# Performance work log

Measured on AMD Instinct MI355X. Metric: run time of the kernel, lower is better.

Reference implementation:

```python
import jax, jax.numpy as jnp
import numpy as np

# Production-scale graph dims (see shape_source)
N = 50000      # nodes
E = 800000     # edges (avg degree 16)
C_IN = 128     # input feature dim
H = 96         # hidden (per species: prey X and predator Y)
C_OUT = 40     # num_classes
L = 5          # LVConv layers
DT = 0.05      # integration step


def setup_inputs() -> dict:
    key = jax.random.key(0)
    ks = jax.random.split(key, 14)
    x = jax.random.normal(ks[0], (N, C_IN), jnp.float32)
    edge_index = jax.random.randint(ks[1], (2, E), 0, N, dtype=jnp.int32)
    # lift linears
    Wx = jax.random.normal(ks[2], (C_IN, H), jnp.float32) / np.sqrt(C_IN)
    bx = jnp.zeros((H,), jnp.float32)
    Wy = jax.random.normal(ks[3], (C_IN, H), jnp.float32) / np.sqrt(C_IN)
    by = jnp.zeros((H,), jnp.float32)
    # per-layer Lotka-Volterra coefficients (per-channel), small positive scale
    alpha = 0.1 * jax.random.uniform(ks[4], (L, H), jnp.float32)
    beta  = 0.1 * jax.random.uniform(ks[5], (L, H), jnp.float32)
    gamma = 0.1 * jax.random.uniform(ks[6], (L, H), jnp.float32)
    delta = 0.1 * jax.random.uniform(ks[7], (L, H), jnp.float32)
    # readout on concat([X, Y])
    Wr = jax.random.normal(ks[8], (2 * H, C_OUT), jnp.float32) / np.sqrt(2 * H)
    br = jnp.zeros((C_OUT,), jnp.float32)
    return {"x": x, "edge_index": edge_index, "Wx": Wx, "bx": bx,
            "Wy": Wy, "by": by, "alpha": alpha, "beta": beta,
            "gamma": gamma, "delta": delta, "Wr": Wr, "br": br}


def reference(x, edge_index, Wx, bx, Wy, by, alpha, beta, gamma, delta, Wr, br):
    src, dst = edge_index[0], edge_index[1]
    # in-degree for mean aggregation over incoming edges
    deg = jax.ops.segment_sum(jnp.ones((E,), x.dtype), dst, num_segments=N)
    deg_inv = (1.0 / jnp.maximum(deg, 1.0))[:, None]  # [N,1]

    def mean_agg(v):  # [N,H] -> [N,H] neighbor mean (src -> dst)
        return jax.ops.segment_sum(v[src], dst, num_segments=N) * deg_inv

    # lift to prey (X) and predator (Y) populations
    X = jnp.tanh(x @ Wx + bx)
    Y = jnp.tanh(x @ Wy + by)
    # dropout is identity in eval mode (training=False)
    for l in range(L):
        aggX = mean_agg(X)
        aggY = mean_agg(Y)
        # explicit-Euler Lotka-Volterra dynamics on the graph
        Xn = X + DT * X * (alpha[l] - beta[l] * aggY)
        Yn = Y + DT * Y * (-gamma[l] + delta[l] * aggX)
        X, Y = Xn, Yn
    h = jnp.concatenate([X, Y], axis=-1)  # [N, 2H]
    return h @ Wr + br
```

## Files before the change

kernel.cpp:

```cpp
#include <hip/hip_runtime.h>
#include <hip/hip_bf16.h>
#include <hip/hip_fp16.h>


#define HDIM 96
#define CIN 128
#define COUT 40
#define NLAYER 5
#define DTC 0.05f

#define BK_SHIFT 7
#define BK_SIZE 128
#define EPB 2048
#define BCAP 3072
#define BSTRIDE 3584

typedef float  vfloat2 __attribute__((ext_vector_type(2)));
typedef float  vfloat4 __attribute__((ext_vector_type(4)));
typedef short  vshort8 __attribute__((ext_vector_type(8)));

__device__ __forceinline__ unsigned bf16_rne(float f) {
    unsigned u = __float_as_uint(f);
    return (u + 0x7fffu + ((u >> 16) & 1u)) >> 16;
}

__device__ __forceinline__ unsigned pack_bf16_pair(float xf, float yf) {
    return bf16_rne(xf) | (bf16_rne(yf) << 16);
}

__device__ __forceinline__ unsigned pack_f16_pair(float a, float b) {
    unsigned ha = (unsigned)__half_as_ushort(__float2half_rn(a));
    unsigned hb = (unsigned)__half_as_ushort(__float2half_rn(b));
    return ha | (hb << 16);
}

__device__ __forceinline__ float f16_lo(unsigned u) {
    return __half2float(__ushort_as_half((unsigned short)(u & 0xffffu)));
}
__device__ __forceinline__ float f16_hi(unsigned u) {
    return __half2float(__ushort_as_half((unsigned short)(u >> 16)));
}

__device__ __forceinline__ unsigned pack_fp8_quad(float x0, float y0, float x1, float y1) {
    int lo = __builtin_amdgcn_cvt_pk_fp8_f32(x0, y0, 0, false);
    int full = __builtin_amdgcn_cvt_pk_fp8_f32(x1, y1, lo, true);
    return (unsigned)full;
}

__device__ __forceinline__ float fast_tanh(float x) {
    float e = __expf(2.0f * x);
    return 1.0f - 2.0f * __builtin_amdgcn_rcpf(e + 1.0f);
}


__global__ __launch_bounds__(256) void wprep_kernel(
    const float* __restrict__ Wx, const float* __restrict__ bx,
    const float* __restrict__ Wy, const float* __restrict__ by,
    unsigned short* __restrict__ WcT, float* __restrict__ bc,
    int* __restrict__ gcur, int NB,
    unsigned* __restrict__ F0, unsigned* __restrict__ F1, int N) {
    int t = blockIdx.x * blockDim.x + threadIdx.x;
    if (t < NB) gcur[t] = 0;
    if (t < 192 * 128) {
        int cc = t >> 7;
        int k = t & 127;
        int h = cc >> 1;
        float w = (cc & 1) ? Wy[k * HDIM + h] : Wx[k * HDIM + h];
        WcT[cc * 128 + k] = (unsigned short)bf16_rne(w);
    }
    if (t < 192) {
        int h = t >> 1;
        bc[t] = (t & 1) ? by[h] : bx[h];
    }
    if (blockIdx.x == 0 && threadIdx.x < 48) {
        int plane = threadIdx.x >> 4, d = threadIdx.x & 15;
        size_t o = ((size_t)plane * (N + 1) + N) * 16 + d;
        F0[o] = 0u;
        F1[o] = 0u;
    }
}


__global__ __launch_bounds__(256) void bscatter_kernel(
    const int* __restrict__ src, const int* __restrict__ dst,
    int* __restrict__ gcur, unsigned* __restrict__ packed, int E, int NB) {
    __shared__ int h[512];
    __shared__ int cur[512];
    for (int i = threadIdx.x; i < NB; i += 256) h[i] = 0;
    __syncthreads();
    int base = blockIdx.x * EPB;
    int end = min(E, base + EPB);
    for (int e = base + threadIdx.x; e < end; e += 256)
        atomicAdd(&h[dst[e] >> BK_SHIFT], 1);
    __syncthreads();
    for (int i = threadIdx.x; i < NB; i += 256)
        cur[i] = h[i] ? atomicAdd(&gcur[i], h[i]) : 0;
    __syncthreads();
    for (int e = base + threadIdx.x; e < end; e += 256) {
        int d = dst[e];
        int b = d >> BK_SHIFT;
        int pos = atomicAdd(&cur[b], 1);
        if (pos < BCAP)
            packed[(size_t)b * BCAP + pos] =
                (unsigned)src[e] | ((unsigned)(d & (BK_SIZE - 1)) << 17);
    }
}


__global__ __launch_bounds__(256) void bcsr_kernel(
    const unsigned* __restrict__ packed, const int* __restrict__ gcur,
    uint2* __restrict__ rowinfo, int* __restrict__ csr, int N, int NB) {
    __shared__ int ldeg[BK_SIZE];
    __shared__ int sscan[BK_SIZE];
    __shared__ int lcur[BK_SIZE];
    int b = blockIdx.x;
    int t = threadIdx.x;
    int cnt = min(gcur[b], BCAP);
    const unsigned* pk = packed + (size_t)b * BCAP;
    int wbase = b * BSTRIDE;
    if (t < BK_SIZE) ldeg[t] = 0;
    __syncthreads();
    for (int e = t; e < cnt; e += 256)
        atomicAdd(&ldeg[(pk[e] >> 17) & (BK_SIZE - 1)], 1);
    __syncthreads();
    int deg = 0, pad = 0;
    if (t < BK_SIZE) {
        deg = ldeg[t];
        pad = (deg + 3) & ~3;
        sscan[t] = pad;
    }
    __syncthreads();
    for (int off = 1; off < BK_SIZE; off <<= 1) {
        int tv = (t < BK_SIZE && t >= off) ? sscan[t - off] : 0;
        __syncthreads();
        if (t < BK_SIZE) sscan[t] += tv;
        __syncthreads();
    }
    int gpos = 0;
    if (t < BK_SIZE) {
        gpos = wbase + sscan[t] - pad;
        lcur[t] = gpos;
        int node = b * BK_SIZE + t;
        if (node < N) {
            rowinfo[node] = make_uint2(
                (unsigned)gpos | ((unsigned)(pad >> 2) << 21),
                __float_as_uint(1.0f / fmaxf((float)deg, 1.0f)));
        }
    }
    __syncthreads();
    for (int e = t; e < cnt; e += 256) {
        unsigned p = pk[e];
        int l = (p >> 17) & (BK_SIZE - 1);
        int pos = atomicAdd(&lcur[l], 1);
        csr[pos] = (int)(p & 0x1FFFFu);
    }
    __syncthreads();
    if (t < BK_SIZE) {
        for (int p = lcur[t]; p < gpos + pad; p++) csr[p] = N;
    }
}


#define LW_STRIDE 136
#define TILE_STRIDE 200

__global__ __launch_bounds__(256) void lift_mfma_kernel(
    const float* __restrict__ x, const unsigned short* __restrict__ WcT,
    const float* __restrict__ bc, unsigned* __restrict__ S,
    unsigned* __restrict__ F, int N) {
    __shared__ __align__(16) char smem[192 * LW_STRIDE * 2];
    __shared__ float sBc[192];
    unsigned short* sW = (unsigned short*)smem;
    unsigned short* tile = (unsigned short*)smem;
    int t = threadIdx.x;

    {
        const unsigned* g = (const unsigned*)WcT;
        unsigned* s = (unsigned*)sW;
        for (int i = t; i < 192 * 64; i += 256) {
            int cc = i >> 6;
            int kp = i & 63;
            s[cc * (LW_STRIDE / 2) + kp] = g[i];
        }
    }
    if (t < 192) sBc[t] = bc[t];
    __syncthreads();

    int wv = t >> 6;
    int lane = t & 63;
    int quad = lane >> 4;
    int m = lane & 15;
    int mbase = blockIdx.x * 64 + wv * 16;

    int anode = mbase + m;
    if (anode >= N) anode = N - 1;
    const float* xrow = x + (size_t)anode * CIN;

    vfloat4 acc[12];
#pragma unroll
    for (int i = 0; i < 12; i++) acc[i] = (vfloat4){0.f, 0.f, 0.f, 0.f};

#pragma unroll
    for (int kt = 0; kt < 4; kt++) {
        int k0 = kt * 32 + quad * 8;
        float4 xa = *(const float4*)(xrow + k0);
        float4 xb = *(const float4*)(xrow + k0 + 4);
        uint4 ua;
        ua.x = pack_bf16_pair(xa.x, xa.y);
        ua.y = pack_bf16_pair(xa.z, xa.w);
        ua.z = pack_bf16_pair(xb.x, xb.y);
        ua.w = pack_bf16_pair(xb.z, xb.w);
        vshort8 a = *(vshort8*)&ua;
#pragma unroll
        for (int nt = 0; nt < 12; nt++) {
            vshort8 b = *(const vshort8*)&sW[(nt * 16 + m) * LW_STRIDE + k0];
            acc[nt] = __builtin_amdgcn_mfma_f32_16x16x32_bf16(a, b, acc[nt], 0, 0, 0);
        }
    }

    __syncthreads();
#pragma unroll
    for (int nt = 0; nt < 12; nt++) {
        int ccb = nt * 16 + m;
        float bco = sBc[ccb];
#pragma unroll
        for (int r = 0; r < 4; r++) {
            int nl = wv * 16 + quad * 4 + r;
            float v = fast_tanh(acc[nt][r] + bco);
            tile[nl * TILE_STRIDE + ccb] = __half_as_ushort(__float2half_rn(v));
        }
    }
    __syncthreads();

    int nbase = blockIdx.x * 64;
#pragma unroll
    for (int i = 0; i < 6; i++) {
        int idx = i * 256 + t;
        int nl = idx / 24;
        int pos = idx - nl * 24;
        int node = nbase + nl;
        uint4 u = *(const uint4*)&tile[nl * TILE_STRIDE + pos * 8];
        if (node < N) {
            *(uint4*)(S + (size_t)node * 96 + pos * 4) = u;
            float f0 = f16_lo(u.x), f1 = f16_hi(u.x);
            float f2 = f16_lo(u.y), f3 = f16_hi(u.y);
            float f4 = f16_lo(u.z), f5 = f16_hi(u.z);
            float f6 = f16_lo(u.w), f7 = f16_hi(u.w);
            uint2 fq = make_uint2(pack_fp8_quad(f0, f1, f2, f3),
                                  pack_fp8_quad(f4, f5, f6, f7));
            int plane = pos >> 3;
            int slot = (2 * pos) & 15;
            *(uint2*)(F + ((size_t)plane * (N + 1) + node) * 16 + slot) = fq;
        }
    }
}


__global__ __launch_bounds__(256) void layer_kernel(
    const unsigned* __restrict__ F, const unsigned* __restrict__ S,
    unsigned* __restrict__ Sn, unsigned* __restrict__ Fn,
    const uint2* __restrict__ rowinfo, const int* __restrict__ csr,
    const float* __restrict__ alpha, const float* __restrict__ beta,
    const float* __restrict__ gamma, const float* __restrict__ delta,
    int N, int nblk) {
    int bid = blockIdx.x;
    int plane = bid / nblk;
    int tile = bid - plane * nblk;
    size_t pstride = (size_t)(N + 1) * 16;
    const unsigned* Fp = F + (size_t)plane * pstride;

    int wave = threadIdx.x >> 6;
    int lane = threadIdx.x & 63;
    int li = lane & 15;
    int gbase = lane & 48;

    int node = (tile * 4 + wave) * 4 + (lane >> 4);
    bool nvalid = node < N;
    int nclamp = nvalid ? node : N - 1;
    uint2 ri = rowinfo[nclamp];
    int beg = (int)(ri.x & 0x1FFFFFu);
    int cnt = nvalid ? (int)((ri.x >> 21) << 2) : 0;
    float dinv = __uint_as_float(ri.y);

    vfloat2 a0 = (vfloat2){0.f, 0.f};
    vfloat2 a1 = (vfloat2){0.f, 0.f};

#define UNP(u)                                                              \
    do {                                                                    \
        a0 += __builtin_amdgcn_cvt_pk_f32_fp8((int)(u), false);             \
        a1 += __builtin_amdgcn_cvt_pk_f32_fp8((int)(u), true);              \
    } while (0)

    for (int base = 0; base < cnt; base += 64) {
        int rem = min(cnt - base, 64);
        int4 my = {0, 0, 0, 0};
        if (li * 4 < rem) my = *(const int4*)(csr + beg + base + 4 * li);
        int j = 0;
        for (; j + 8 <= rem; j += 8) {
            int l0 = gbase + (j >> 2);
            int s0 = __shfl(my.x, l0);
            int s1 = __shfl(my.y, l0);
            int s2 = __shfl(my.z, l0);
            int s3 = __shfl(my.w, l0);
            int s4 = __shfl(my.x, l0 + 1);
            int s5 = __shfl(my.y, l0 + 1);
            int s6 = __shfl(my.z, l0 + 1);
            int s7 = __shfl(my.w, l0 + 1);
            unsigned u0 = Fp[(size_t)s0 * 16 + li];
            unsigned u1 = Fp[(size_t)s1 * 16 + li];
            unsigned u2 = Fp[(size_t)s2 * 16 + li];
            unsigned u3 = Fp[(size_t)s3 * 16 + li];
            unsigned u4 = Fp[(size_t)s4 * 16 + li];
            unsigned u5 = Fp[(size_t)s5 * 16 + li];
            unsigned u6 = Fp[(size_t)s6 * 16 + li];
            unsigned u7 = Fp[(size_t)s7 * 16 + li];
            UNP(u0); UNP(u1); UNP(u2); UNP(u3);
            UNP(u4); UNP(u5); UNP(u6); UNP(u7);
        }
        if (j < rem) {
            int l0 = gbase + (j >> 2);
            int s0 = __shfl(my.x, l0);
            int s1 = __shfl(my.y, l0);
            int s2 = __shfl(my.z, l0);
            int s3 = __shfl(my.w, l0);
            unsigned u0 = Fp[(size_t)s0 * 16 + li];
            unsigned u1 = Fp[(size_t)s1 * 16 + li];
            unsigned u2 = Fp[(size_t)s2 * 16 + li];
            unsigned u3 = Fp[(size_t)s3 * 16 + li];
            UNP(u0); UNP(u1); UNP(u2); UNP(u3);
        }
    }
#undef UNP

    if (!nvalid) return;

    int h0 = plane * 32 + 2 * li;
    float2 a2 = *(const float2*)(alpha + h0);
    float2 b2 = *(const float2*)(beta + h0);
    float2 g2 = *(const float2*)(gamma + h0);
    float2 d2 = *(const float2*)(delta + h0);
    uint2 su = *(const uint2*)(S + (size_t)node * 96 + h0);
    float vx = f16_lo(su.x), vy = f16_hi(su.x);
    float vz = f16_lo(su.y), vw = f16_hi(su.y);
    float ox = vx + DTC * vx * (a2.x - b2.x * (a0.y * dinv));
    float oy = vy + DTC * vy * (-g2.x + d2.x * (a0.x * dinv));
    float oz = vz + DTC * vz * (a2.y - b2.y * (a1.y * dinv));
    float ow = vw + DTC * vw * (-g2.y + d2.y * (a1.x * dinv));
    uint2 so = make_uint2(pack_f16_pair(ox, oy), pack_f16_pair(oz, ow));
    *(uint2*)(Sn + (size_t)node * 96 + h0) = so;
    if (Fn) Fn[(size_t)plane * pstride + (size_t)node * 16 + li] =
        pack_fp8_quad(ox, oy, oz, ow);
}


#define WG_STRIDE 200

__global__ __launch_bounds__(256) void readout_mfma_kernel(
    const unsigned short* __restrict__ sh, const float* __restrict__ Wr,
    const float* __restrict__ br, float* __restrict__ out, int N) {
    __shared__ unsigned short sW[48 * WG_STRIDE];
    __shared__ float sB[48];
    int t = threadIdx.x;

    for (int i = t; i < 48 * 192; i += 256) {
        int n = i / 192;
        int kk = i - n * 192;
        int h = kk >> 1;
        float w = 0.f;
        if (n < COUT) w = (kk & 1) ? Wr[(HDIM + h) * COUT + n] : Wr[h * COUT + n];
        sW[n * WG_STRIDE + kk] = __half_as_ushort(__float2half_rn(w));
    }
    if (t < 48) sB[t] = (t < COUT) ? br[t] : 0.f;
    __syncthreads();

    int wv = t >> 6;
    int lane = t & 63;
    int quad = lane >> 4;
    int m = lane & 15;
    int mbase = blockIdx.x * 64 + wv * 16;

    int anode = mbase + m;
    if (anode >= N) anode = N - 1;
    const unsigned short* arow = sh + (size_t)anode * 192;

    vfloat4 acc0 = {0.f, 0.f, 0.f, 0.f};
    vfloat4 acc1 = {0.f, 0.f, 0.f, 0.f};
    vfloat4 acc2 = {0.f, 0.f, 0.f, 0.f};

#pragma unroll
    for (int kt = 0; kt < 6; kt++) {
        int k0 = kt * 32 + quad * 8;
        vshort8 a = *(const vshort8*)(arow + k0);
        vshort8 b0 = *(const vshort8*)&sW[(0 * 16 + m) * WG_STRIDE + k0];
        vshort8 b1 = *(const vshort8*)&sW[(1 * 16 + m) * WG_STRIDE + k0];
        vshort8 b2 = *(const vshort8*)&sW[(2 * 16 + m) * WG_STRIDE + k0];
        acc0 = __builtin_amdgcn_mfma_f32_16x16x32_f16(a, b0, acc0, 0, 0, 0);
        acc1 = __builtin_amdgcn_mfma_f32_16x16x32_f16(a, b1, acc1, 0, 0, 0);
        acc2 = __builtin_amdgcn_mfma_f32_16x16x32_f16(a, b2, acc2, 0, 0, 0);
    }

    float bo0 = sB[m];
    float bo1 = sB[16 + m];
    float bo2 = (m < 8) ? sB[32 + m] : 0.f;
#pragma unroll
    for (int r = 0; r < 4; r++) {
        int node = mbase + quad * 4 + r;
        if (node < N) {
            float* orow = out + (size_t)node * COUT;
            orow[m] = acc0[r] + bo0;
            orow[16 + m] = acc1[r] + bo1;
            if (m < 8) orow[32 + m] = acc2[r] + bo2;
        }
    }
}


extern "C" void kernel_launch(void* const* d_in, const int* in_sizes, int n_in,
                              void* d_out, int out_size, void* d_ws, size_t ws_size,
                              hipStream_t stream) {
    const float* x     = (const float*)d_in[0];
    const int*   ei    = (const int*)d_in[1];
    const float* Wx    = (const float*)d_in[2];
    const float* bx    = (const float*)d_in[3];
    const float* Wy    = (const float*)d_in[4];
    const float* by    = (const float*)d_in[5];
    const float* alpha = (const float*)d_in[6];
    const float* beta  = (const float*)d_in[7];
    const float* gamma = (const float*)d_in[8];
    const float* delta = (const float*)d_in[9];
    const float* Wr    = (const float*)d_in[10];
    const float* br    = (const float*)d_in[11];

    const int N = in_sizes[0] / CIN;
    const int E = in_sizes[1] / 2;
    const int NB = (N + BK_SIZE - 1) >> BK_SHIFT;
    const int nchunk = (E + EPB - 1) / EPB;
    const int nblk = (N + 15) / 16;

    char* ws = (char*)d_ws;
    size_t off = 0;
    auto alloc = [&](size_t bytes) -> void* {
        off = (off + 255) & ~(size_t)255;
        void* p = ws + off;
        off += bytes;
        return p;
    };
    int* gcur          = (int*)alloc((size_t)NB * sizeof(int));
    unsigned* pckd     = (unsigned*)alloc((size_t)NB * BCAP * sizeof(unsigned));
    uint2* rowinfo     = (uint2*)alloc((size_t)N * sizeof(uint2));
    int* csr           = (int*)alloc(((size_t)NB * BSTRIDE + 64) * sizeof(int));
    unsigned* Sa   = (unsigned*)alloc((size_t)N * 96 * sizeof(unsigned));
    unsigned* Sb   = (unsigned*)alloc((size_t)N * 96 * sizeof(unsigned));
    unsigned* Fa   = (unsigned*)alloc((size_t)(N + 1) * 48 * sizeof(unsigned));
    unsigned* Fb   = (unsigned*)alloc((size_t)(N + 1) * 48 * sizeof(unsigned));
    unsigned short* WcT = (unsigned short*)alloc((size_t)192 * 128 * sizeof(unsigned short));
    float* bc      = (float*)alloc((size_t)192 * sizeof(float));
    (void)ws_size;

    const int* e_src = ei;
    const int* e_dst = ei + E;

    wprep_kernel<<<(192 * 128 + 255) / 256, 256, 0, stream>>>(
        Wx, bx, Wy, by, WcT, bc, gcur, NB, Fa, Fb, N);

    bscatter_kernel<<<nchunk, 256, 0, stream>>>(e_src, e_dst, gcur, pckd, E, NB);
    bcsr_kernel<<<NB, 256, 0, stream>>>(pckd, gcur, rowinfo, csr, N, NB);

    lift_mfma_kernel<<<(N + 63) / 64, 256, 0, stream>>>(x, WcT, bc, Sa, Fa, N);

    const unsigned* Sc = Sa;
    unsigned* Snx = Sb;
    const unsigned* Fc = Fa;
    unsigned* Fnx = Fb;
    for (int l = 0; l < NLAYER; l++) {
        bool last = (l == NLAYER - 1);
        layer_kernel<<<3 * nblk, 256, 0, stream>>>(
            Fc, Sc, Snx, last ? (unsigned*)nullptr : Fnx,
            rowinfo, csr,
            alpha + l * HDIM, beta + l * HDIM, gamma + l * HDIM, delta + l * HDIM,
            N, nblk);
        const unsigned* ts = Sc; Sc = Snx; Snx = (unsigned*)ts;
        const unsigned* tf = Fc; Fc = Fnx; Fnx = (unsigned*)tf;
    }

    readout_mfma_kernel<<<(N + 63) / 64, 256, 0, stream>>>(
        (const unsigned short*)Sc, Wr, br, (float*)d_out, N);
}
```

Measured before the change: 285.3 us.

## Use 16-bit CSR indices and 8-lane-per-node gathers with in-place state update

Neighbour indices are stored as unsigned shorts, and rows are padded to multiples of 8 so each node reads one 16-byte vector of 8 indices per step with no cross-lane shuffles. Each node is now handled by 8 lanes, each gathering 8 bytes of fp8 features per neighbour, so fewer load instructions are issued per edge and each block covers 32 nodes. The f16 state buffer is updated in place, which drops the second state buffer and its ping-pong. The 16-bit indices only hold for fewer than 65536 nodes, and padding to 8 adds some dummy gathers.

```diff
diff --git a/kernel.cpp b/kernel.cpp
--- a/kernel.cpp
+++ b/kernel.cpp
@@ -13,7 +13,7 @@
 #define BK_SIZE 128
 #define EPB 2048
 #define BCAP 3072
-#define BSTRIDE 3584
+#define BSTRIDE 4096
 
 typedef float  vfloat2 __attribute__((ext_vector_type(2)));
 typedef float  vfloat4 __attribute__((ext_vector_type(4)));
@@ -109,7 +109,7 @@
 
 __global__ __launch_bounds__(256) void bcsr_kernel(
     const unsigned* __restrict__ packed, const int* __restrict__ gcur,
-    uint2* __restrict__ rowinfo, int* __restrict__ csr, int N, int NB) {
+    uint2* __restrict__ rowinfo, unsigned short* __restrict__ csr, int N, int NB) {
     __shared__ int ldeg[BK_SIZE];
     __shared__ int sscan[BK_SIZE];
     __shared__ int lcur[BK_SIZE];
@@ -126,7 +126,7 @@
     int deg = 0, pad = 0;
     if (t < BK_SIZE) {
         deg = ldeg[t];
-        pad = (deg + 3) & ~3;
+        pad = (deg + 7) & ~7;
         sscan[t] = pad;
     }
     __syncthreads();
@@ -152,11 +152,11 @@
         unsigned p = pk[e];
         int l = (p >> 17) & (BK_SIZE - 1);
         int pos = atomicAdd(&lcur[l], 1);
-        csr[pos] = (int)(p & 0x1FFFFu);
+        csr[pos] = (unsigned short)(p & 0x1FFFFu);
     }
     __syncthreads();
     if (t < BK_SIZE) {
-        for (int p = lcur[t]; p < gpos + pad; p++) csr[p] = N;
+        for (int p = lcur[t]; p < gpos + pad; p++) csr[p] = (unsigned short)N;
     }
 }
 
@@ -257,99 +257,101 @@
 
 
 __global__ __launch_bounds__(256) void layer_kernel(
-    const unsigned* __restrict__ F, const unsigned* __restrict__ S,
-    unsigned* __restrict__ Sn, unsigned* __restrict__ Fn,
-    const uint2* __restrict__ rowinfo, const int* __restrict__ csr,
+    const unsigned* __restrict__ F, unsigned* __restrict__ S,
+    unsigned* __restrict__ Fn,
+    const uint2* __restrict__ rowinfo, const unsigned short* __restrict__ csr,
     const float* __restrict__ alpha, const float* __restrict__ beta,
     const float* __restrict__ gamma, const float* __restrict__ delta,
     int N, int nblk) {
     int bid = blockIdx.x;
     int plane = bid / nblk;
     int tile = bid - plane * nblk;
-    size_t pstride = (size_t)(N + 1) * 16;
+    unsigned pstride = (unsigned)(N + 1) * 16u;
     const unsigned* Fp = F + (size_t)plane * pstride;
 
     int wave = threadIdx.x >> 6;
     int lane = threadIdx.x & 63;
-    int li = lane & 15;
-    int gbase = lane & 48;
-
-    int node = (tile * 4 + wave) * 4 + (lane >> 4);
+    int li = lane & 7;
+    unsigned tli = (unsigned)(2 * li);
+
+    int node = tile * 32 + wave * 8 + (lane >> 3);
     bool nvalid = node < N;
     int nclamp = nvalid ? node : N - 1;
     uint2 ri = rowinfo[nclamp];
-    int beg = (int)(ri.x & 0x1FFFFFu);
+    unsigned beg = ri.x & 0x1FFFFFu;
     int cnt = nvalid ? (int)((ri.x >> 21) << 2) : 0;
     float dinv = __uint_as_float(ri.y);
 
-    vfloat2 a0 = (vfloat2){0.f, 0.f};
-    vfloat2 a1 = (vfloat2){0.f, 0.f};
+    vfloat2 a0 = {0.f, 0.f}, a1 = {0.f, 0.f}, a2 = {0.f, 0.f}, a3 = {0.f, 0.f};
 
 #define UNP(u)                                                              \
     do {                                                                    \
-        a0 += __builtin_amdgcn_cvt_pk_f32_fp8((int)(u), false);             \
-        a1 += __builtin_amdgcn_cvt_pk_f32_fp8((int)(u), true);              \
+        a0 += __builtin_amdgcn_cvt_pk_f32_fp8((int)(u).x, false);           \
+        a1 += __builtin_amdgcn_cvt_pk_f32_fp8((int)(u).x, true);            \
+        a2 += __builtin_amdgcn_cvt_pk_f32_fp8((int)(u).y, false);           \
+        a3 += __builtin_amdgcn_cvt_pk_f32_fp8((int)(u).y, true);            \
     } while (0)
 
-    for (int base = 0; base < cnt; base += 64) {
-        int rem = min(cnt - base, 64);
-        int4 my = {0, 0, 0, 0};
-        if (li * 4 < rem) my = *(const int4*)(csr + beg + base + 4 * li);
-        int j = 0;
-        for (; j + 8 <= rem; j += 8) {
-            int l0 = gbase + (j >> 2);
-            int s0 = __shfl(my.x, l0);
-            int s1 = __shfl(my.y, l0);
-            int s2 = __shfl(my.z, l0);
-            int s3 = __shfl(my.w, l0);
-            int s4 = __shfl(my.x, l0 + 1);
-            int s5 = __shfl(my.y, l0 + 1);
-            int s6 = __shfl(my.z, l0 + 1);
-            int s7 = __shfl(my.w, l0 + 1);
-            unsigned u0 = Fp[(size_t)s0 * 16 + li];
-            unsigned u1 = Fp[(size_t)s1 * 16 + li];
-            unsigned u2 = Fp[(size_t)s2 * 16 + li];
-            unsigned u3 = Fp[(size_t)s3 * 16 + li];
-            unsigned u4 = Fp[(size_t)s4 * 16 + li];
-            unsigned u5 = Fp[(size_t)s5 * 16 + li];
-            unsigned u6 = Fp[(size_t)s6 * 16 + li];
-            unsigned u7 = Fp[(size_t)s7 * 16 + li];
-            UNP(u0); UNP(u1); UNP(u2); UNP(u3);
-            UNP(u4); UNP(u5); UNP(u6); UNP(u7);
-        }
-        if (j < rem) {
-            int l0 = gbase + (j >> 2);
-            int s0 = __shfl(my.x, l0);
-            int s1 = __shfl(my.y, l0);
-            int s2 = __shfl(my.z, l0);
-            int s3 = __shfl(my.w, l0);
-            unsigned u0 = Fp[(size_t)s0 * 16 + li];
-            unsigned u1 = Fp[(size_t)s1 * 16 + li];
-            unsigned u2 = Fp[(size_t)s2 * 16 + li];
-            unsigned u3 = Fp[(size_t)s3 * 16 + li];
-            UNP(u0); UNP(u1); UNP(u2); UNP(u3);
-        }
+    for (int j = 0; j < cnt; j += 8) {
+        uint4 w = *(const uint4*)(csr + beg + (unsigned)j);
+        unsigned o0 = ((w.x & 0xffffu) << 4) + tli;
+        unsigned o1 = ((w.x >> 16) << 4) + tli;
+        unsigned o2 = ((w.y & 0xffffu) << 4) + tli;
+        unsigned o3 = ((w.y >> 16) << 4) + tli;
+        unsigned o4 = ((w.z & 0xffffu) << 4) + tli;
+        unsigned o5 = ((w.z >> 16) << 4) + tli;
+        unsigned o6 = ((w.w & 0xffffu) << 4) + tli;
+        unsigned o7 = ((w.w >> 16) << 4) + tli;
+        uint2 u0 = *(const uint2*)(Fp + o0);
+        uint2 u1 = *(const uint2*)(Fp + o1);
+        uint2 u2 = *(const uint2*)(Fp + o2);
+        uint2 u3 = *(const uint2*)(Fp + o3);
+        uint2 u4 = *(const uint2*)(Fp + o4);
+        uint2 u5 = *(const uint2*)(Fp + o5);
+        uint2 u6 = *(const uint2*)(Fp + o6);
+        uint2 u7 = *(const uint2*)(Fp + o7);
+        UNP(u0); UNP(u1); UNP(u2); UNP(u3);
+        UNP(u4); UNP(u5); UNP(u6); UNP(u7);
     }
 #undef UNP
 
     if (!nvalid) return;
 
-    int h0 = plane * 32 + 2 * li;
-    float2 a2 = *(const float2*)(alpha + h0);
-    float2 b2 = *(const float2*)(beta + h0);
-    float2 g2 = *(const float2*)(gamma + h0);
-    float2 d2 = *(const float2*)(delta + h0);
-    uint2 su = *(const uint2*)(S + (size_t)node * 96 + h0);
-    float vx = f16_lo(su.x), vy = f16_hi(su.x);
-    float vz = f16_lo(su.y), vw = f16_hi(su.y);
-    float ox = vx + DTC * vx * (a2.x - b2.x * (a0.y * dinv));
-    float oy = vy + DTC * vy * (-g2.x + d2.x * (a0.x * dinv));
-    float oz = vz + DTC * vz * (a2.y - b2.y * (a1.y * dinv));
-    float ow = vw + DTC * vw * (-g2.y + d2.y * (a1.x * dinv));
-    uint2 so = make_uint2(pack_f16_pair(ox, oy), pack_f16_pair(oz, ow));
-    *(uint2*)(Sn + (size_t)node * 96 + h0) = so;
-    if (Fn) Fn[(size_t)plane * pstride + (size_t)node * 16 + li] =
-        pack_fp8_quad(ox, oy, oz, ow);
+    int h0 = plane * 32 + 4 * li;
+    float4 av = *(const float4*)(alpha + h0);
+    float4 bv = *(const float4*)(beta + h0);
+    float4 gv = *(const float4*)(gamma + h0);
+    float4 dv = *(const float4*)(delta + h0);
+    unsigned* srow = S + (size_t)node * 96 + h0;
+    uint4 su = *(const uint4*)srow;
+
+    float x0 = f16_lo(su.x), y0 = f16_hi(su.x);
+    float x1 = f16_lo(su.y), y1 = f16_hi(su.y);
+    float x2 = f16_lo(su.z), y2 = f16_hi(su.z);
+    float x3 = f16_lo(su.w), y3 = f16_hi(su.w);
+
+    float ox0 = x0 + DTC * x0 * (av.x - bv.x * (a0.y * dinv));
+    float oy0 = y0 + DTC * y0 * (-gv.x + dv.x * (a0.x * dinv));
+    float ox1 = x1 + DTC * x1 * (av.y - bv.y * (a1.y * dinv));
+    float oy1 = y1 + DTC * y1 * (-gv.y + dv.y * (a1.x * dinv));
+    float ox2 = x2 + DTC * x2 * (av.z - bv.z * (a2.y * dinv));
+    float oy2 = y2 + DTC * y2 * (-gv.z + dv.z * (a2.x * dinv));
+    float ox3 = x3 + DTC * x3 * (av.w - bv.w * (a3.y * dinv));
+    float oy3 = y3 + DTC * y3 * (-gv.w + dv.w * (a3.x * dinv));
+
+    uint4 so;
+    so.x = pack_f16_pair(ox0, oy0);
+    so.y = pack_f16_pair(ox1, oy1);
+    so.z = pack_f16_pair(ox2, oy2);
+    so.w = pack_f16_pair(ox3, oy3);
+    *(uint4*)srow = so;
+
+    if (Fn) {
+        uint2 fo;
+        fo.x = pack_fp8_quad(ox0, oy0, ox1, oy1);
+        fo.y = pack_fp8_quad(ox2, oy2, ox3, oy3);
+        *(uint2*)(Fn + (size_t)plane * pstride + (unsigned)node * 16u + tli) = fo;
+    }
 }
 
 
@@ -435,7 +437,7 @@
     const int E = in_sizes[1] / 2;
     const int NB = (N + BK_SIZE - 1) >> BK_SHIFT;
     const int nchunk = (E + EPB - 1) / EPB;
-    const int nblk = (N + 15) / 16;
+    const int nblk = (N + 31) / 32;
 
     char* ws = (char*)d_ws;
     size_t off = 0;
@@ -448,9 +450,8 @@
     int* gcur          = (int*)alloc((size_t)NB * sizeof(int));
     unsigned* pckd     = (unsigned*)alloc((size_t)NB * BCAP * sizeof(unsigned));
     uint2* rowinfo     = (uint2*)alloc((size_t)N * sizeof(uint2));
-    int* csr           = (int*)alloc(((size_t)NB * BSTRIDE + 64) * sizeof(int));
+    unsigned short* csr = (unsigned short*)alloc(((size_t)NB * BSTRIDE + 64) * sizeof(unsigned short));
     unsigned* Sa   = (unsigned*)alloc((size_t)N * 96 * sizeof(unsigned));
-    unsigned* Sb   = (unsigned*)alloc((size_t)N * 96 * sizeof(unsigned));
     unsigned* Fa   = (unsigned*)alloc((size_t)(N + 1) * 48 * sizeof(unsigned));
     unsigned* Fb   = (unsigned*)alloc((size_t)(N + 1) * 48 * sizeof(unsigned));
     unsigned short* WcT = (unsigned short*)alloc((size_t)192 * 128 * sizeof(unsigned short));
@@ -468,21 +469,18 @@
 
     lift_mfma_kernel<<<(N + 63) / 64, 256, 0, stream>>>(x, WcT, bc, Sa, Fa, N);
 
-    const unsigned* Sc = Sa;
-    unsigned* Snx = Sb;
     const unsigned* Fc = Fa;
     unsigned* Fnx = Fb;
     for (int l = 0; l < NLAYER; l++) {
         bool last = (l == NLAYER - 1);
         layer_kernel<<<3 * nblk, 256, 0, stream>>>(
-            Fc, Sc, Snx, last ? (unsigned*)nullptr : Fnx,
+            Fc, Sa, last ? (unsigned*)nullptr : Fnx,
             rowinfo, csr,
             alpha + l * HDIM, beta + l * HDIM, gamma + l * HDIM, delta + l * HDIM,
             N, nblk);
-        const unsigned* ts = Sc; Sc = Snx; Snx = (unsigned*)ts;
         const unsigned* tf = Fc; Fc = Fnx; Fnx = (unsigned*)tf;
     }
 
     readout_mfma_kernel<<<(N + 63) / 64, 256, 0, stream>>>(
-        (const unsigned short*)Sc, Wr, br, (float*)d_out, N);
-}
+        (const unsigned short*)Sa, Wr, br, (float*)d_out, N);
+}
```

Result: no change. 290.2 us (+1.7%).
